# Kernel tuning notes

Hardware: AMD Instinct MI355X
Metric: run time of the kernel (lower is better)

The kernel has to match this reference:

```python
import jax, jax.numpy as jnp
import numpy as np

B, S, HID = 2, 2048, 4096
NH, NKV, D = 32, 8, 128
GROUPS = NH // NKV  # 4 query heads per KV head
THETA = 10000.0
MAX_SEQ = 4096


def _rope_tables():
    half = D // 2
    inv_freq = 1.0 / (THETA ** (np.arange(half, dtype=np.float32) / half))
    t = np.arange(MAX_SEQ, dtype=np.float32)
    freqs = np.outer(t, inv_freq)  # [MAX_SEQ, D//2]
    return jnp.asarray(np.cos(freqs)), jnp.asarray(np.sin(freqs))

ROPE_COS, ROPE_SIN = _rope_tables()


def _apply_rope(x, cos, sin):
    # x: [B, S, H, D]; cos/sin: [S, D//2]; half-split (NeoX) rotation as in _apply_rope_inline
    half = x.shape[-1] // 2
    x0, x1 = x[..., :half], x[..., half:]
    c = cos[None, :, None, :]
    s = sin[None, :, None, :]
    return jnp.concatenate([x0 * c - x1 * s, x0 * s + x1 * c], axis=-1)


def setup_inputs() -> dict:
    key = jax.random.key(0)
    ks = jax.random.split(key, 5)
    wscale = 1.0 / np.sqrt(HID).astype(np.float32)  # keep activations O(1)
    return {
        "x": jax.random.normal(ks[0], (B, S, HID), dtype=jnp.float32),
        "positions": jnp.arange(S, dtype=jnp.int32),
        "w_q": jax.random.normal(ks[1], (NH * D, HID), dtype=jnp.float32) * wscale,
        "w_k": jax.random.normal(ks[2], (NKV * D, HID), dtype=jnp.float32) * wscale,
        "w_v": jax.random.normal(ks[3], (NKV * D, HID), dtype=jnp.float32) * wscale,
        "w_o": jax.random.normal(ks[4], (HID, NH * D), dtype=jnp.float32) * wscale,
    }


def reference(x, positions, w_q, w_k, w_v, w_o):
    cos = ROPE_COS[positions]  # [S, D//2]
    sin = ROPE_SIN[positions]
    # Separate Q/K/V projections (no bias), as in the training forward()
    q = (x @ w_q.T).reshape(B, S, NH, D)
    k = (x @ w_k.T).reshape(B, S, NKV, D)
    v = (x @ w_v.T).reshape(B, S, NKV, D)
    q = _apply_rope(q, cos, sin)
    k = _apply_rope(k, cos, sin)
    # [B, H, S, D] layout
    q = q.transpose(0, 2, 1, 3)
    k = k.transpose(0, 2, 1, 3)
    v = v.transpose(0, 2, 1, 3)
    # GQA: group query heads over shared KV heads instead of repeating K/V
    qg = q.reshape(B, NKV, GROUPS, S, D)
    scale = 1.0 / jnp.sqrt(jnp.float32(D))
    scores = jnp.einsum("bkgqd,bkmd->bkgqm", qg, k) * scale  # [B, NKV, G, Sq, Skv]
    causal = jnp.tril(jnp.ones((S, S), dtype=bool))
    scores = jnp.where(causal[None, None, None], scores, jnp.float32(-jnp.inf))
    probs = jax.nn.softmax(scores, axis=-1)
    ctx = jnp.einsum("bkgqm,bkmd->bkgqd", probs, v)  # [B, NKV, G, S, D]
    ctx = ctx.reshape(B, NH, S, D).transpose(0, 2, 1, 3).reshape(B, S, NH * D)
    return ctx @ w_o.T
```

## Files before the change

### kernel.cpp

```cpp
#include <hip/hip_runtime.h>
#include <math.h>

typedef short s16x8 __attribute__((ext_vector_type(8)));
typedef float f32x4 __attribute__((ext_vector_type(4)));
typedef unsigned u32x4 __attribute__((ext_vector_type(4)));
typedef unsigned short u16;

#define S_LEN 2048
#define HID_DIM 4096
#define NH_Q 32
#define NKV_H 8
#define DHEAD 128

__device__ __forceinline__ u16 f2bf(float f) {
  unsigned u = __builtin_bit_cast(unsigned, f);
  u += 0x7fffu + ((u >> 16) & 1u);
  return (u16)(u >> 16);
}

__device__ __forceinline__ void gload16(const u16* g, u16* l) {
  __builtin_amdgcn_global_load_lds(
      (const __attribute__((address_space(1))) void*)g,
      (__attribute__((address_space(3))) void*)l, 16, 0, 0);
}

__global__ void cvt_kernel(const float* __restrict__ in, u16* __restrict__ out, int n4) {
  int stride = gridDim.x * blockDim.x;
  for (int i = blockIdx.x * blockDim.x + threadIdx.x; i < n4; i += stride) {
    float4 f = ((const float4*)in)[i];
    uint2 o;
    o.x = (unsigned)f2bf(f.x) | ((unsigned)f2bf(f.y) << 16);
    o.y = (unsigned)f2bf(f.z) | ((unsigned)f2bf(f.w) << 16);
    ((uint2*)out)[i] = o;
  }
}

__global__ void cvt_all_kernel(const float* __restrict__ x, const float* __restrict__ wq,
                               const float* __restrict__ wk, const float* __restrict__ wv,
                               const float* __restrict__ wo, u16* __restrict__ x_bf,
                               u16* __restrict__ wqkv_bf, u16* __restrict__ wo_bf,
                               int with_wo) {
  const int R0 = 4194304, R1 = 8388608, R2 = 9437184, R3 = 10485760, R4 = 14680064;
  const int total = with_wo ? R4 : R3;
  const int stride = gridDim.x * blockDim.x;
  for (int i = blockIdx.x * blockDim.x + threadIdx.x; i < total; i += stride) {
    const float* src;
    u16* dst;
    int off;
    if (i < R0)      { src = x;  dst = x_bf;               off = i; }
    else if (i < R1) { src = wq; dst = wqkv_bf;            off = i - R0; }
    else if (i < R2) { src = wk; dst = wqkv_bf + 16777216; off = i - R1; }
    else if (i < R3) { src = wv; dst = wqkv_bf + 20971520; off = i - R2; }
    else             { src = wo; dst = wo_bf;              off = i - R3; }
    float4 f = ((const float4*)src)[off];
    uint2 o;
    o.x = (unsigned)f2bf(f.x) | ((unsigned)f2bf(f.y) << 16);
    o.y = (unsigned)f2bf(f.z) | ((unsigned)f2bf(f.w) << 16);
    ((uint2*)dst)[off] = o;
  }
}

__global__ void rope_table_kernel(const int* __restrict__ positions,
                                  float* __restrict__ cos_t, float* __restrict__ sin_t) {
  int idx = blockIdx.x * 256 + threadIdx.x;
  if (idx >= S_LEN * 64) return;
  int s = idx >> 6, j = idx & 63;
  float pos = (float)positions[s];
  float inv = expf(-(float)j * (9.210340371976184f / 64.0f));
  float ang = pos * inv;
  float sv, cv;
  sincosf(ang, &sv, &cv);
  cos_t[idx] = cv;
  sin_t[idx] = sv;
}

template<int EPI>
__global__ __launch_bounds__(512, 2) void gemm8ph_kernel(
    const u16* __restrict__ A, const u16* __restrict__ B,
    void* __restrict__ outp, int M, int N, int K,
    const float* __restrict__ cos_t, const float* __restrict__ sin_t) {
  __shared__ u16 LDS[65536];
  const int t = threadIdx.x;
  const int wave = t >> 6, lane = t & 63;
  const int l15 = lane & 15, lhi = lane >> 4;
  const int wr = wave >> 2, wc = wave & 3;
  const int gx = gridDim.x;
  const int nwg = gx * gridDim.y;
  const int id = blockIdx.y * gx + blockIdx.x;
  const int swz = (id & 7) * (nwg >> 3) + (id >> 3);
  const int bm = (swz / gx) * 256, bn = (swz % gx) * 256;

  const int sw = l15 & 7;
  int aoff[4][2], boff[2][2];
#pragma unroll
  for (int q = 0; q < 4; ++q)
#pragma unroll
    for (int ks = 0; ks < 2; ++ks)
      aoff[q][ks] = (wr * 64 + q * 16 + l15) * 64 + (((ks << 2) + lhi) ^ sw) * 8;
#pragma unroll
  for (int f = 0; f < 2; ++f)
#pragma unroll
    for (int ks = 0; ks < 2; ++ks)
      boff[f][ks] = (f * 64 + wc * 16 + l15) * 64 + (((ks << 2) + lhi) ^ sw) * 8;

  const int lr1 = t >> 3;
  const int cs1 = ((t & 7) ^ (lr1 & 7)) * 8;
  const int rA1 = lr1;
  const int rA2 = 128 + lr1;
  const int ldsw = wave * 512;

  const f32x4 fz = {0.f, 0.f, 0.f, 0.f};
  f32x4 acc[8][4];
#pragma unroll
  for (int mf = 0; mf < 8; ++mf)
#pragma unroll
    for (int nf = 0; nf < 4; ++nf) acc[mf][nf] = fz;

  auto stageA = [&](int tile, int h, int buf) {
    const size_t kb = (size_t)tile * 64;
    gload16(A + (size_t)(bm + h * 64 + rA1) * K + kb + cs1,
            &LDS[buf * 16384 + h * 8192 + ldsw]);
    gload16(A + (size_t)(bm + h * 64 + rA2) * K + kb + cs1,
            &LDS[buf * 16384 + h * 8192 + 4096 + ldsw]);
  };
  auto stageB = [&](int tile, int h, int buf) {
    const size_t kb = (size_t)tile * 64;
    gload16(B + (size_t)(bn + h * 128 + lr1) * K + kb + cs1,
            &LDS[32768 + buf * 16384 + h * 8192 + ldsw]);
    gload16(B + (size_t)(bn + h * 128 + 64 + lr1) * K + kb + cs1,
            &LDS[32768 + buf * 16384 + h * 8192 + 4096 + ldsw]);
  };

  s16x8 afr[4][2], bfr[2][2], bfrK[2][2];
  auto readA = [&](int mfH, int buf) {
    const int base = buf * 16384 + mfH * 8192;
#pragma unroll
    for (int q = 0; q < 4; ++q)
#pragma unroll
      for (int ks = 0; ks < 2; ++ks)
        afr[q][ks] = *(const s16x8*)&LDS[base + aoff[q][ks]];
  };
  auto readB = [&](int nfH, int buf, s16x8 (&dst)[2][2]) {
    const int base = 32768 + buf * 16384 + nfH * 8192;
#pragma unroll
    for (int f = 0; f < 2; ++f)
#pragma unroll
      for (int ks = 0; ks < 2; ++ks)
        dst[f][ks] = *(const s16x8*)&LDS[base + boff[f][ks]];
  };
  auto mfma16 = [&](int mfH, int nfH, const s16x8 (&bb)[2][2]) {
    __builtin_amdgcn_s_setprio(1);
#pragma unroll
    for (int q = 0; q < 4; ++q)
#pragma unroll
      for (int f = 0; f < 2; ++f)
#pragma unroll
        for (int ks = 0; ks < 2; ++ks)
          acc[mfH * 4 + q][nfH * 2 + f] = __builtin_amdgcn_mfma_f32_16x16x32_bf16(
              afr[q][ks], bb[f][ks], acc[mfH * 4 + q][nfH * 2 + f], 0, 0, 0);
    __builtin_amdgcn_s_setprio(0);
  };

#define PHASE_SYNC()                        \
  do {                                      \
    __builtin_amdgcn_s_barrier();           \
    asm volatile("s_waitcnt lgkmcnt(0)");   \
    __builtin_amdgcn_sched_barrier(0);      \
  } while (0)

  stageA(0, 0, 0); stageB(0, 0, 0); stageB(0, 1, 0); stageA(0, 1, 0);
  stageA(1, 0, 1); stageB(1, 0, 1); stageB(1, 1, 1);
  asm volatile("s_waitcnt vmcnt(6)");
  __builtin_amdgcn_sched_barrier(0);
  __builtin_amdgcn_s_barrier();

  const int nt = K >> 6;
  for (int i = 0; i < (nt >> 1); ++i) {
    const int u = 2 * i, v = 2 * i + 1;
    const bool s2 = (u + 2) < nt;
    readA(0, 0); readB(0, 0, bfrK); stageA(v, 1, 1);
    PHASE_SYNC(); mfma16(0, 0, bfrK); __builtin_amdgcn_s_barrier();
    readB(1, 0, bfr); if (s2) stageB(u + 2, 0, 0);
    PHASE_SYNC(); mfma16(0, 1, bfr); __builtin_amdgcn_s_barrier();
    readA(1, 0); if (s2) stageB(u + 2, 1, 0);
    PHASE_SYNC(); mfma16(1, 1, bfr); __builtin_amdgcn_s_barrier();
    if (s2) { stageA(u + 2, 0, 0); asm volatile("s_waitcnt vmcnt(6)"); }
    else    { asm volatile("s_waitcnt vmcnt(0)"); }
    PHASE_SYNC(); mfma16(1, 0, bfrK); __builtin_amdgcn_s_barrier();
    readA(0, 1); readB(0, 1, bfrK); if (s2) stageA(u + 2, 1, 0);
    PHASE_SYNC(); mfma16(0, 0, bfrK); __builtin_amdgcn_s_barrier();
    readB(1, 1, bfr); if (s2) stageB(v + 2, 0, 1);
    PHASE_SYNC(); mfma16(0, 1, bfr); __builtin_amdgcn_s_barrier();
    readA(1, 1); if (s2) stageB(v + 2, 1, 1);
    PHASE_SYNC(); mfma16(1, 1, bfr); __builtin_amdgcn_s_barrier();
    if (s2) { stageA(v + 2, 0, 1); asm volatile("s_waitcnt vmcnt(6)"); }
    else    { asm volatile("s_waitcnt vmcnt(0)"); }
    PHASE_SYNC(); mfma16(1, 0, bfrK); __builtin_amdgcn_s_barrier();
  }
#undef PHASE_SYNC

  if constexpr (EPI == 0) {
    float* C = (float*)outp;
#pragma unroll
    for (int mf = 0; mf < 8; ++mf) {
      int rb = bm + wr * 128 + mf * 16 + lhi * 4;
#pragma unroll
      for (int nfi = 0; nfi < 4; ++nfi) {
        int col = bn + wc * 16 + (nfi & 1) * 64 + (nfi >> 1) * 128 + l15;
#pragma unroll
        for (int i = 0; i < 4; ++i) C[(size_t)(rb + i) * N + col] = acc[mf][nfi][i];
      }
    }
  } else {
    u16* qp = (u16*)outp;
    u16* kp = qp + 16777216;
    u16* vp = kp + 4194304;
    if (bn < 5120) {
      const bool isQ = bn < 4096;
      u16* O = isQ ? qp : kp;
      const int hb = isQ ? (bn >> 7) : ((bn - 4096) >> 7);
      const int Hh = isQ ? NH_Q : NKV_H;
      const int j = wc * 16 + l15;
#pragma unroll
      for (int mf = 0; mf < 8; ++mf) {
        int rb = bm + wr * 128 + mf * 16 + lhi * 4;
#pragma unroll
        for (int p = 0; p < 2; ++p) {
          int head = hb + p;
#pragma unroll
          for (int i = 0; i < 4; ++i) {
            int m = rb + i;
            int b = m >> 11, srw = m & 2047;
            float c = cos_t[srw * 64 + j];
            float s = sin_t[srw * 64 + j];
            float x0 = acc[mf][2 * p][i];
            float x1 = acc[mf][2 * p + 1][i];
            size_t base = ((size_t)(b * Hh + head) * S_LEN + srw) * DHEAD;
            O[base + j] = f2bf(x0 * c - x1 * s);
            O[base + j + 64] = f2bf(x0 * s + x1 * c);
          }
        }
      }
    } else {
#pragma unroll
      for (int mf = 0; mf < 8; ++mf) {
        int rb = bm + wr * 128 + mf * 16 + lhi * 4;
#pragma unroll
        for (int nfi = 0; nfi < 4; ++nfi) {
          int colrel = bn - 5120 + wc * 16 + (nfi & 1) * 64 + (nfi >> 1) * 128 + l15;
          int head = colrel >> 7, d = colrel & 127;
#pragma unroll
          for (int i = 0; i < 4; ++i) {
            int m = rb + i;
            int b = m >> 11, srw = m & 2047;
            vp[((size_t)(b * NKV_H + head) * DHEAD + d) * S_LEN + srw] = f2bf(acc[mf][nfi][i]);
          }
        }
      }
    }
  }
}

template<int EPI, bool ABF16, bool BBF16>
__global__ __launch_bounds__(256) void gemm_kernel(
    const void* __restrict__ Aptr, const void* __restrict__ Bptr,
    void* __restrict__ outp, void* __restrict__ outp2, int M, int N, int K,
    const float* __restrict__ cos_t, const float* __restrict__ sin_t, int Hh) {
  __shared__ u16 As[128][72];
  __shared__ u16 Bs[128][72];
  const int t = threadIdx.x;
  const int wave = t >> 6, lane = t & 63;
  const int l15 = lane & 15, lhi = lane >> 4;
  const int gx = gridDim.x;
  const int nwg = gx * gridDim.y;
  const int id = blockIdx.y * gx + blockIdx.x;
  const int swz = (id & 7) * (nwg >> 3) + (id >> 3);
  const int bm = (swz / gx) * 128, bn = (swz % gx) * 128;

  const f32x4 fz = {0.f, 0.f, 0.f, 0.f};
  f32x4 acc[2][8];
#pragma unroll
  for (int a0 = 0; a0 < 2; ++a0)
#pragma unroll
    for (int b0 = 0; b0 < 8; ++b0) acc[a0][b0] = fz;

  for (int kt = 0; kt < K; kt += 64) {
    __syncthreads();
    if (ABF16) {
      const u16* A = (const u16*)Aptr;
#pragma unroll
      for (int p = 0; p < 4; ++p) {
        int row = p * 32 + (t >> 3), kc = (t & 7) * 8;
        *(s16x8*)&As[row][kc] = *(const s16x8*)(A + (size_t)(bm + row) * K + kt + kc);
      }
    } else {
      const float* A = (const float*)Aptr;
#pragma unroll
      for (int p = 0; p < 8; ++p) {
        int row = p * 16 + (t >> 4), kc = (t & 15) * 4;
        float4 f = *(const float4*)(A + (size_t)(bm + row) * K + kt + kc);
        unsigned* dst = (unsigned*)&As[row][kc];
        dst[0] = (unsigned)f2bf(f.x) | ((unsigned)f2bf(f.y) << 16);
        dst[1] = (unsigned)f2bf(f.z) | ((unsigned)f2bf(f.w) << 16);
      }
    }
    if (BBF16) {
      const u16* Bw = (const u16*)Bptr;
#pragma unroll
      for (int p = 0; p < 4; ++p) {
        int row = p * 32 + (t >> 3), kc = (t & 7) * 8;
        *(s16x8*)&Bs[row][kc] = *(const s16x8*)(Bw + (size_t)(bn + row) * K + kt + kc);
      }
    } else {
      const float* Bw = (const float*)Bptr;
#pragma unroll
      for (int p = 0; p < 8; ++p) {
        int row = p * 16 + (t >> 4), kc = (t & 15) * 4;
        float4 f = *(const float4*)(Bw + (size_t)(bn + row) * K + kt + kc);
        unsigned* dst = (unsigned*)&Bs[row][kc];
        dst[0] = (unsigned)f2bf(f.x) | ((unsigned)f2bf(f.y) << 16);
        dst[1] = (unsigned)f2bf(f.z) | ((unsigned)f2bf(f.w) << 16);
      }
    }
    __syncthreads();
#pragma unroll
    for (int ks = 0; ks < 2; ++ks) {
      s16x8 bfr[8];
#pragma unroll
      for (int nf = 0; nf < 8; ++nf)
        bfr[nf] = *(const s16x8*)&Bs[nf * 16 + l15][ks * 32 + lhi * 8];
#pragma unroll
      for (int mf = 0; mf < 2; ++mf) {
        s16x8 a = *(const s16x8*)&As[wave * 32 + mf * 16 + l15][ks * 32 + lhi * 8];
#pragma unroll
        for (int nf = 0; nf < 8; ++nf)
          acc[mf][nf] = __builtin_amdgcn_mfma_f32_16x16x32_bf16(a, bfr[nf], acc[mf][nf], 0, 0, 0);
      }
    }
  }

  if (EPI == 0) {
    float* C = (float*)outp;
#pragma unroll
    for (int mf = 0; mf < 2; ++mf)
#pragma unroll
      for (int nf = 0; nf < 8; ++nf) {
        int col = bn + nf * 16 + l15;
        int rb = bm + wave * 32 + mf * 16 + lhi * 4;
#pragma unroll
        for (int i = 0; i < 4; ++i) C[(size_t)(rb + i) * N + col] = acc[mf][nf][i];
      }
  } else if (EPI == 2) {
    u16* O = (u16*)outp;
    int h = bn >> 7;
#pragma unroll
    for (int mf = 0; mf < 2; ++mf)
#pragma unroll
      for (int nf = 0; nf < 4; ++nf) {
        int j = nf * 16 + l15;
        int rb = bm + wave * 32 + mf * 16 + lhi * 4;
#pragma unroll
        for (int i = 0; i < 4; ++i) {
          int m = rb + i;
          int b = m >> 11, srow = m & 2047;
          float c = cos_t[srow * 64 + j];
          float s = sin_t[srow * 64 + j];
          float x0 = acc[mf][nf][i];
          float x1 = acc[mf][nf + 4][i];
          size_t base = ((size_t)(b * Hh + h) * S_LEN + srow) * DHEAD;
          O[base + j] = f2bf(x0 * c - x1 * s);
          O[base + j + 64] = f2bf(x0 * s + x1 * c);
        }
      }
  } else {
    u16* O = (u16*)outp;
#pragma unroll
    for (int mf = 0; mf < 2; ++mf)
#pragma unroll
      for (int nf = 0; nf < 8; ++nf) {
        int col = bn + nf * 16 + l15;
        int h = col >> 7, d = col & 127;
        int rb = bm + wave * 32 + mf * 16 + lhi * 4;
#pragma unroll
        for (int i = 0; i < 4; ++i) {
          int m = rb + i;
          int b = m >> 11, srow = m & 2047;
          O[((size_t)(b * Hh + h) * DHEAD + d) * S_LEN + srow] = f2bf(acc[mf][nf][i]);
        }
      }
  }
}

#define KIDX(r, c) (((r) * 128 + (c)) ^ (((r) & 7) << 3))
#define VIDX(d, kv) (((d) * 64 + (kv)) ^ (((d) & 7) << 3))
__global__ __launch_bounds__(512) void attn_kernel(
    const u16* __restrict__ q, const u16* __restrict__ k, const u16* __restrict__ vt,
    u16* __restrict__ ctx) {
  __shared__ u16 Ks[64 * 128];
  __shared__ u16 Vts[128 * 64];

  const int t = threadIdx.x;
  const int wave = t >> 6, lane = t & 63;
  const int l15 = lane & 15, lhi = lane >> 4;
  const int pi = blockIdx.x, h = blockIdx.y, b = blockIdx.z;
  const int kvh = h >> 2;
  const int qsub[2] = {pi, 15 - pi};
  const int ntiles = 32 - 2 * pi;

  const u16* qb = q + ((size_t)(b * NH_Q + h)) * S_LEN * DHEAD;
  const u16* kb = k + ((size_t)(b * NKV_H + kvh)) * S_LEN * DHEAD;
  const u16* vtb = vt + ((size_t)(b * NKV_H + kvh)) * DHEAD * S_LEN;
// ... 45 lines not shown
      kr0 = *(const s16x8*)p;
      kr1 = *(const s16x8*)(p + 8);
      const u16* pv = vtb + (size_t)vrow * S_LEN + (tt + 1) * 64 + vk0;
      vr0 = *(const s16x8*)pv;
      vr1 = *(const s16x8*)(pv + 8);
    }

    const int kc_base = tt * 64;
#pragma unroll
    for (int s = 0; s < 2; ++s) {
      const int wmin = qsub[s] * 128 + wave * 16;
      if (kc_base > wmin + 15) continue;
      f32x4 sacc[4];
#pragma unroll
      for (int i = 0; i < 4; ++i) sacc[i] = fz;
      __builtin_amdgcn_s_setprio(1);
#pragma unroll
      for (int ks = 0; ks < 4; ++ks) {
#pragma unroll
        for (int nf = 0; nf < 4; ++nf) {
          s16x8 kf = *(const s16x8*)&Ks[KIDX(nf * 16 + l15, ks * 32 + lhi * 8)];
          sacc[nf] = __builtin_amdgcn_mfma_f32_16x16x32_bf16(kf, qf[s][ks], sacc[nf], 0, 0, 0);
        }
      }
      __builtin_amdgcn_s_setprio(0);

      const int qg = wmin + l15;
      float pmax = -INFINITY;
      if (kc_base + 63 > wmin) {
#pragma unroll
        for (int nf = 0; nf < 4; ++nf)
#pragma unroll
          for (int i = 0; i < 4; ++i) {
            int kv = kc_base + nf * 16 + lhi * 4 + i;
            float sv = sacc[nf][i] * scale;
            sv = (kv <= qg) ? sv : -INFINITY;
            sacc[nf][i] = sv;
            pmax = fmaxf(pmax, sv);
          }
      } else {
#pragma unroll
        for (int nf = 0; nf < 4; ++nf)
#pragma unroll
          for (int i = 0; i < 4; ++i) {
            float sv = sacc[nf][i] * scale;
            sacc[nf][i] = sv;
            pmax = fmaxf(pmax, sv);
          }
      }
      pmax = fmaxf(pmax, __shfl_xor(pmax, 16, 64));
      pmax = fmaxf(pmax, __shfl_xor(pmax, 32, 64));

      if (!__all(pmax <= mrow[s] + 8.0f)) {
        float mnew = fmaxf(mrow[s], pmax);
        float alpha = __expf(mrow[s] - mnew);
        mrow[s] = mnew;
        lsum[s] *= alpha;
#pragma unroll
        for (int i = 0; i < 4; ++i) {
          float al = __shfl(alpha, (lane & 48) | (lhi * 4 + i), 64);
#pragma unroll
          for (int df = 0; df < 8; ++df) acc[s][df][i] *= al;
        }
      }

      float rsum = 0.f;
      unsigned pk[4][2];
#pragma unroll
      for (int nf = 0; nf < 4; ++nf) {
        float p0 = __expf(sacc[nf][0] - mrow[s]);
        float p1 = __expf(sacc[nf][1] - mrow[s]);
        float p2 = __expf(sacc[nf][2] - mrow[s]);
        float p3 = __expf(sacc[nf][3] - mrow[s]);
        rsum += (p0 + p1) + (p2 + p3);
        pk[nf][0] = (unsigned)f2bf(p0) | ((unsigned)f2bf(p1) << 16);
        pk[nf][1] = (unsigned)f2bf(p2) | ((unsigned)f2bf(p3) << 16);
      }
      rsum += __shfl_xor(rsum, 16, 64);
      rsum += __shfl_xor(rsum, 32, 64);
      lsum[s] += rsum;

      s16x8 pa[2];
#pragma unroll
      for (int ph = 0; ph < 2; ++ph) {
        unsigned lo0 = __shfl((int)pk[2 * ph][0], sl0, 64);
        unsigned hi0 = __shfl((int)pk[2 * ph + 1][0], sl0, 64);
        unsigned lo1 = __shfl((int)pk[2 * ph][1], sl0, 64);
        unsigned hi1 = __shfl((int)pk[2 * ph + 1][1], sl0, 64);
        unsigned lo2 = __shfl((int)pk[2 * ph][0], sl1, 64);
        unsigned hi2 = __shfl((int)pk[2 * ph + 1][0], sl1, 64);
        unsigned lo3 = __shfl((int)pk[2 * ph][1], sl1, 64);
        unsigned hi3 = __shfl((int)pk[2 * ph + 1][1], sl1, 64);
        u32x4 w;
        w[0] = hisel ? hi0 : lo0;
        w[1] = hisel ? hi1 : lo1;
        w[2] = hisel ? hi2 : lo2;
        w[3] = hisel ? hi3 : lo3;
        pa[ph] = __builtin_bit_cast(s16x8, w);
      }

      __builtin_amdgcn_s_setprio(1);
#pragma unroll
      for (int ph = 0; ph < 2; ++ph) {
#pragma unroll
        for (int df = 0; df < 8; ++df) {
          s16x8 bb = *(const s16x8*)&Vts[VIDX(df * 16 + l15, ph * 32 + lhi * 8)];
          acc[s][df] = __builtin_amdgcn_mfma_f32_16x16x32_bf16(pa[ph], bb, acc[s][df], 0, 0, 0);
        }
      }
      __builtin_amdgcn_s_setprio(0);
    }
  }

#pragma unroll
  for (int s = 0; s < 2; ++s) {
    float rl = 1.0f / lsum[s];
#pragma unroll
    for (int i = 0; i < 4; ++i) {
      float rli = __shfl(rl, (lane & 48) | (lhi * 4 + i), 64);
      int m = b * S_LEN + qsub[s] * 128 + wave * 16 + lhi * 4 + i;
#pragma unroll
      for (int df = 0; df < 8; ++df) {
        int col = h * DHEAD + df * 16 + l15;
        ctx[(size_t)m * (NH_Q * DHEAD) + col] = f2bf(acc[s][df][i] * rli);
      }
    }
  }
}

extern "C" void kernel_launch(void* const* d_in, const int* in_sizes, int n_in,
                              void* d_out, int out_size, void* d_ws, size_t ws_size,
                              hipStream_t stream) {
  const float* x = (const float*)d_in[0];
  const int* positions = (const int*)d_in[1];
  const float* wq = (const float*)d_in[2];
  const float* wk = (const float*)d_in[3];
  const float* wv = (const float*)d_in[4];
  const float* wo = (const float*)d_in[5];
  float* out = (float*)d_out;

  char* ws = (char*)d_ws;
  const size_t MB1 = 1048576;
  const size_t SZ_X = 33554432;
  const size_t SZ_WQKV = 50331648;
  const size_t SZ_WO = 33554432;
  const size_t SZ_Q = 33554432;
  const size_t SZ_WK = 8388608;
  const size_t NEED_FULL = MB1 + SZ_X + SZ_WQKV + SZ_Q + 2 * SZ_WK;
  const size_t NEED_WO = NEED_FULL + SZ_WO;

  float* cos_t = (float*)ws;
  float* sin_t = (float*)(ws + MB1 / 2);

  rope_table_kernel<<<512, 256, 0, stream>>>(positions, cos_t, sin_t);

  if (ws_size >= NEED_WO) {
    char* p = ws + MB1;
    u16* x_bf = (u16*)p;    p += SZ_X;
    u16* wqkv_bf = (u16*)p; p += SZ_WQKV;
    u16* wo_bf = (u16*)p;   p += SZ_WO;
    u16* q_ws = (u16*)p;    p += SZ_Q;
    u16* k_ws = (u16*)p;    p += SZ_WK;
    u16* v_ws = (u16*)p;    p += SZ_WK;
    u16* ctx_ws = x_bf;

    cvt_all_kernel<<<2048, 256, 0, stream>>>(x, wq, wk, wv, wo, x_bf, wqkv_bf, wo_bf, 1);
    gemm8ph_kernel<5><<<dim3(24, 16), 512, 0, stream>>>(
        x_bf, wqkv_bf, q_ws, 4096, 6144, 4096, cos_t, sin_t);
    attn_kernel<<<dim3(8, 32, 2), 512, 0, stream>>>(q_ws, k_ws, v_ws, ctx_ws);
    gemm8ph_kernel<0><<<dim3(16, 16), 512, 0, stream>>>(
        ctx_ws, wo_bf, out, 4096, 4096, 4096, nullptr, nullptr);
  } else if (ws_size >= NEED_FULL) {
    char* p = ws + MB1;
    u16* x_bf = (u16*)p;    p += SZ_X;
    u16* wqkv_bf = (u16*)p; p += SZ_WQKV;
    u16* q_ws = (u16*)p;    p += SZ_Q;
    u16* k_ws = (u16*)p;    p += SZ_WK;
    u16* v_ws = (u16*)p;    p += SZ_WK;
    u16* ctx_ws = x_bf;

    cvt_all_kernel<<<2048, 256, 0, stream>>>(x, wq, wk, wv, nullptr, x_bf, wqkv_bf, nullptr, 0);
    gemm8ph_kernel<5><<<dim3(24, 16), 512, 0, stream>>>(
        x_bf, wqkv_bf, q_ws, 4096, 6144, 4096, cos_t, sin_t);
    cvt_kernel<<<2048, 256, 0, stream>>>(wo, wqkv_bf, 4194304);
    attn_kernel<<<dim3(8, 32, 2), 512, 0, stream>>>(q_ws, k_ws, v_ws, ctx_ws);
    gemm8ph_kernel<0><<<dim3(16, 16), 512, 0, stream>>>(
        ctx_ws, wqkv_bf, out, 4096, 4096, 4096, nullptr, nullptr);
  } else {
    u16* q_ws = (u16*)(ws + MB1);
    u16* k_ws = (u16*)(ws + MB1 + SZ_Q);
    u16* v_ws = (u16*)(ws + MB1 + SZ_Q + SZ_WK);
    u16* ctx_ws = (u16*)(ws + MB1 + SZ_Q + 2 * SZ_WK);

    gemm_kernel<2, false, false><<<dim3(32, 32), 256, 0, stream>>>(
        x, wq, q_ws, nullptr, 4096, 4096, 4096, cos_t, sin_t, NH_Q);
    gemm_kernel<2, false, false><<<dim3(8, 32), 256, 0, stream>>>(
        x, wk, k_ws, nullptr, 4096, 1024, 4096, cos_t, sin_t, NKV_H);
    gemm_kernel<4, false, false><<<dim3(8, 32), 256, 0, stream>>>(
        x, wv, v_ws, nullptr, 4096, 1024, 4096, nullptr, nullptr, NKV_H);
    attn_kernel<<<dim3(8, 32, 2), 512, 0, stream>>>(q_ws, k_ws, v_ws, ctx_ws);
    gemm_kernel<0, true, false><<<dim3(32, 32), 256, 0, stream>>>(
        ctx_ws, wo, out, nullptr, 4096, 4096, 4096, nullptr, nullptr, 0);
  }
}
```

Before: 537.1 us.

## Use 128x256-tile QKV GEMM kernel and fold RoPE table into conversion

Adds a dedicated QKV projection kernel that uses 128x256 output tiles with a three-stage LDS ring buffer, replacing the 256x256 eight-phase kernel. This doubles the grid to 768 workgroups so the MI355X compute units get a fuller wave of work. The RoPE cos/sin table generation moves into the bf16 conversion kernel, removing one launch. In exchange, smaller tiles give less operand reuse per workgroup and raise global/LDS traffic per FLOP.

New measurement: 525.3 us. 2.2% less time.

```diff
diff --git a/kernel.cpp b/kernel.cpp
--- a/kernel.cpp
+++ b/kernel.cpp
@@ -39,24 +39,42 @@
                                const float* __restrict__ wk, const float* __restrict__ wv,
                                const float* __restrict__ wo, u16* __restrict__ x_bf,
                                u16* __restrict__ wqkv_bf, u16* __restrict__ wo_bf,
-                               int with_wo) {
+                               const int* __restrict__ positions, float* __restrict__ cos_t,
+                               float* __restrict__ sin_t, int with_wo) {
   const int R0 = 4194304, R1 = 8388608, R2 = 9437184, R3 = 10485760, R4 = 14680064;
-  const int total = with_wo ? R4 : R3;
+  const int cvt_end = with_wo ? R4 : R3;
+  const int rope_units = 32768;
+  const int total = cvt_end + rope_units;
   const int stride = gridDim.x * blockDim.x;
   for (int i = blockIdx.x * blockDim.x + threadIdx.x; i < total; i += stride) {
-    const float* src;
-    u16* dst;
-    int off;
-    if (i < R0)      { src = x;  dst = x_bf;               off = i; }
-    else if (i < R1) { src = wq; dst = wqkv_bf;            off = i - R0; }
-    else if (i < R2) { src = wk; dst = wqkv_bf + 16777216; off = i - R1; }
-    else if (i < R3) { src = wv; dst = wqkv_bf + 20971520; off = i - R2; }
-    else             { src = wo; dst = wo_bf;              off = i - R3; }
-    float4 f = ((const float4*)src)[off];
-    uint2 o;
-    o.x = (unsigned)f2bf(f.x) | ((unsigned)f2bf(f.y) << 16);
-    o.y = (unsigned)f2bf(f.z) | ((unsigned)f2bf(f.w) << 16);
-    ((uint2*)dst)[off] = o;
+    if (i < cvt_end) {
+      const float* src;
+      u16* dst;
+      int off;
+      if (i < R0)      { src = x;  dst = x_bf;               off = i; }
+      else if (i < R1) { src = wq; dst = wqkv_bf;            off = i - R0; }
+      else if (i < R2) { src = wk; dst = wqkv_bf + 16777216; off = i - R1; }
+      else if (i < R3) { src = wv; dst = wqkv_bf + 20971520; off = i - R2; }
+      else             { src = wo; dst = wo_bf;              off = i - R3; }
+      float4 f = ((const float4*)src)[off];
+      uint2 o;
+      o.x = (unsigned)f2bf(f.x) | ((unsigned)f2bf(f.y) << 16);
+      o.y = (unsigned)f2bf(f.z) | ((unsigned)f2bf(f.w) << 16);
+      ((uint2*)dst)[off] = o;
+    } else {
+      int base = (i - cvt_end) * 4;
+#pragma unroll
+      for (int e = 0; e < 4; ++e) {
+        int idx = base + e;
+        int s = idx >> 6, j = idx & 63;
+        float pos = (float)positions[s];
+        float inv = expf(-(float)j * (9.210340371976184f / 64.0f));
+        float sv, cv;
+        sincosf(pos * inv, &sv, &cv);
+        cos_t[idx] = cv;
+        sin_t[idx] = sv;
+      }
+    }
   }
 }
 
@@ -67,18 +85,174 @@
   int s = idx >> 6, j = idx & 63;
   float pos = (float)positions[s];
   float inv = expf(-(float)j * (9.210340371976184f / 64.0f));
-  float ang = pos * inv;
   float sv, cv;
-  sincosf(ang, &sv, &cv);
+  sincosf(pos * inv, &sv, &cv);
   cos_t[idx] = cv;
   sin_t[idx] = sv;
 }
 
-template<int EPI>
-__global__ __launch_bounds__(512, 2) void gemm8ph_kernel(
+__global__ __launch_bounds__(512, 2) void gemmq_kernel(
     const u16* __restrict__ A, const u16* __restrict__ B,
     void* __restrict__ outp, int M, int N, int K,
     const float* __restrict__ cos_t, const float* __restrict__ sin_t) {
+  __shared__ u16 LDS[73728];
+  const int t = threadIdx.x;
+  const int wave = t >> 6, lane = t & 63;
+  const int l15 = lane & 15, lhi = lane >> 4;
+  const int wr = wave >> 2, wc = wave & 3;
+  const int gx = gridDim.x;
+  const int nwg = gx * gridDim.y;
+  const int id = blockIdx.y * gx + blockIdx.x;
+  const int swz = (id & 7) * (nwg >> 3) + (id >> 3);
+  const int bm = (swz / gx) * 128, bn = (swz % gx) * 256;
+
+  const int sw = l15 & 7;
+  int aoff[4][2], boff[2][2];
+#pragma unroll
+  for (int q = 0; q < 4; ++q)
+#pragma unroll
+    for (int ks = 0; ks < 2; ++ks)
+      aoff[q][ks] = wr * 4096 + (q * 16 + l15) * 64 + (((ks << 2) + lhi) ^ sw) * 8;
+#pragma unroll
+  for (int f = 0; f < 2; ++f)
+#pragma unroll
+    for (int ks = 0; ks < 2; ++ks)
+      boff[f][ks] = (f * 64 + wc * 16 + l15) * 64 + (((ks << 2) + lhi) ^ sw) * 8;
+
+  const int lr1 = t >> 3;
+  const int cs1 = ((t & 7) ^ (lr1 & 7)) * 8;
+  const int ldsw = wave * 512;
+
+  const f32x4 fz = {0.f, 0.f, 0.f, 0.f};
+  f32x4 acc[4][4];
+#pragma unroll
+  for (int mf = 0; mf < 4; ++mf)
+#pragma unroll
+    for (int nf = 0; nf < 4; ++nf) acc[mf][nf] = fz;
+
+  auto stageA = [&](int tile, int buf) {
+    const size_t kb = (size_t)tile * 64;
+    gload16(A + (size_t)(bm + lr1) * K + kb + cs1, &LDS[buf * 8192 + ldsw]);
+    gload16(A + (size_t)(bm + 64 + lr1) * K + kb + cs1, &LDS[buf * 8192 + 4096 + ldsw]);
+  };
+  auto stageB = [&](int tile, int h, int buf) {
+    const size_t kb = (size_t)tile * 64;
+    gload16(B + (size_t)(bn + h * 128 + lr1) * K + kb + cs1,
+            &LDS[24576 + buf * 16384 + h * 8192 + ldsw]);
+    gload16(B + (size_t)(bn + h * 128 + 64 + lr1) * K + kb + cs1,
+            &LDS[24576 + buf * 16384 + h * 8192 + 4096 + ldsw]);
+  };
+
+  s16x8 afr[4][2], bfr[2][2];
+  auto readA = [&](int buf) {
+    const int base = buf * 8192;
+#pragma unroll
+    for (int q = 0; q < 4; ++q)
+#pragma unroll
+      for (int ks = 0; ks < 2; ++ks)
+        afr[q][ks] = *(const s16x8*)&LDS[base + aoff[q][ks]];
+  };
+  auto readB = [&](int nfH, int buf) {
+    const int base = 24576 + buf * 16384 + nfH * 8192;
+#pragma unroll
+    for (int f = 0; f < 2; ++f)
+#pragma unroll
+      for (int ks = 0; ks < 2; ++ks)
+        bfr[f][ks] = *(const s16x8*)&LDS[base + boff[f][ks]];
+  };
+  auto mfma16 = [&](int nfH) {
+    __builtin_amdgcn_s_setprio(1);
+#pragma unroll
+    for (int q = 0; q < 4; ++q)
+#pragma unroll
+      for (int f = 0; f < 2; ++f)
+#pragma unroll
+        for (int ks = 0; ks < 2; ++ks)
+          acc[q][nfH * 2 + f] = __builtin_amdgcn_mfma_f32_16x16x32_bf16(
+              afr[q][ks], bfr[f][ks], acc[q][nfH * 2 + f], 0, 0, 0);
+    __builtin_amdgcn_s_setprio(0);
+  };
+
+#define PHASE_SYNC()                        \
+  do {                                      \
+    __builtin_amdgcn_s_barrier();           \
+    asm volatile("s_waitcnt lgkmcnt(0)");   \
+    __builtin_amdgcn_sched_barrier(0);      \
+  } while (0)
+
+  stageA(0, 0); stageB(0, 0, 0); stageB(0, 1, 0);
+  stageA(1, 1); stageB(1, 0, 1); stageB(1, 1, 1);
+  asm volatile("s_waitcnt vmcnt(6)");
+  __builtin_amdgcn_sched_barrier(0);
+  __builtin_amdgcn_s_barrier();
+
+  const int nt = K >> 6;
+  int cur = 0, nx2 = 2;
+  for (int tt = 0; tt < nt; ++tt) {
+    const bool s2 = (tt + 2) < nt;
+    readA(cur); readB(0, cur);
+    if (s2) { stageA(tt + 2, nx2); stageB(tt + 2, 0, nx2); }
+    PHASE_SYNC(); mfma16(0); __builtin_amdgcn_s_barrier();
+    readB(1, cur);
+    if (s2) { stageB(tt + 2, 1, nx2); asm volatile("s_waitcnt vmcnt(6)"); }
+    else    { asm volatile("s_waitcnt vmcnt(0)"); }
+    PHASE_SYNC(); mfma16(1); __builtin_amdgcn_s_barrier();
+    cur = (cur == 2) ? 0 : cur + 1;
+    nx2 = (nx2 == 2) ? 0 : nx2 + 1;
+  }
+#undef PHASE_SYNC
+
+  u16* qp = (u16*)outp;
+  u16* kp = qp + 16777216;
+  u16* vp = kp + 4194304;
+  if (bn < 5120) {
+    const bool isQ = bn < 4096;
+    u16* O = isQ ? qp : kp;
+    const int hb = isQ ? (bn >> 7) : ((bn - 4096) >> 7);
+    const int Hh = isQ ? NH_Q : NKV_H;
+    const int j = wc * 16 + l15;
+#pragma unroll
+    for (int mf = 0; mf < 4; ++mf) {
+      int rb = bm + wr * 64 + mf * 16 + lhi * 4;
+#pragma unroll
+      for (int p = 0; p < 2; ++p) {
+        int head = hb + p;
+#pragma unroll
+        for (int i = 0; i < 4; ++i) {
+          int m = rb + i;
+          int b = m >> 11, srw = m & 2047;
+          float c = cos_t[srw * 64 + j];
+          float s = sin_t[srw * 64 + j];
+          float x0 = acc[mf][2 * p][i];
+          float x1 = acc[mf][2 * p + 1][i];
+          size_t base = ((size_t)(b * Hh + head) * S_LEN + srw) * DHEAD;
+          O[base + j] = f2bf(x0 * c - x1 * s);
+          O[base + j + 64] = f2bf(x0 * s + x1 * c);
+        }
+      }
+    }
+  } else {
+#pragma unroll
+    for (int mf = 0; mf < 4; ++mf) {
+      int rb = bm + wr * 64 + mf * 16 + lhi * 4;
+#pragma unroll
+      for (int nfi = 0; nfi < 4; ++nfi) {
+        int colrel = bn - 5120 + wc * 16 + (nfi & 1) * 64 + (nfi >> 1) * 128 + l15;
+        int head = colrel >> 7, d = colrel & 127;
+#pragma unroll
+        for (int i = 0; i < 4; ++i) {
+          int m = rb + i;
+          int b = m >> 11, srw = m & 2047;
+          vp[((size_t)(b * NKV_H + head) * DHEAD + d) * S_LEN + srw] = f2bf(acc[mf][nfi][i]);
+        }
+      }
+    }
+  }
+}
+
+__global__ __launch_bounds__(512, 2) void gemm8ph_kernel(
+    const u16* __restrict__ A, const u16* __restrict__ B,
+    void* __restrict__ outp, int M, int N, int K) {
   __shared__ u16 LDS[65536];
   const int t = threadIdx.x;
   const int wave = t >> 6, lane = t & 63;
@@ -199,64 +373,15 @@
   }
 #undef PHASE_SYNC
 
-  if constexpr (EPI == 0) {
-    float* C = (float*)outp;
-#pragma unroll
-    for (int mf = 0; mf < 8; ++mf) {
-      int rb = bm + wr * 128 + mf * 16 + lhi * 4;
-#pragma unroll
-      for (int nfi = 0; nfi < 4; ++nfi) {
-        int col = bn + wc * 16 + (nfi & 1) * 64 + (nfi >> 1) * 128 + l15;
-#pragma unroll
-        for (int i = 0; i < 4; ++i) C[(size_t)(rb + i) * N + col] = acc[mf][nfi][i];
-      }
-    }
-  } else {
-    u16* qp = (u16*)outp;
-    u16* kp = qp + 16777216;
-    u16* vp = kp + 4194304;
-    if (bn < 5120) {
-      const bool isQ = bn < 4096;
-      u16* O = isQ ? qp : kp;
-      const int hb = isQ ? (bn >> 7) : ((bn - 4096) >> 7);
-      const int Hh = isQ ? NH_Q : NKV_H;
-      const int j = wc * 16 + l15;
-#pragma unroll
-      for (int mf = 0; mf < 8; ++mf) {
-        int rb = bm + wr * 128 + mf * 16 + lhi * 4;
-#pragma unroll
-        for (int p = 0; p < 2; ++p) {
-          int head = hb + p;
-#pragma unroll
-          for (int i = 0; i < 4; ++i) {
-            int m = rb + i;
-            int b = m >> 11, srw = m & 2047;
-            float c = cos_t[srw * 64 + j];
-            float s = sin_t[srw * 64 + j];
-            float x0 = acc[mf][2 * p][i];
-            float x1 = acc[mf][2 * p + 1][i];
-            size_t base = ((size_t)(b * Hh + head) * S_LEN + srw) * DHEAD;
-            O[base + j] = f2bf(x0 * c - x1 * s);
-            O[base + j + 64] = f2bf(x0 * s + x1 * c);
-          }
-        }
-      }
-    } else {
-#pragma unroll
-      for (int mf = 0; mf < 8; ++mf) {
-        int rb = bm + wr * 128 + mf * 16 + lhi * 4;
-#pragma unroll
-        for (int nfi = 0; nfi < 4; ++nfi) {
-          int colrel = bn - 5120 + wc * 16 + (nfi & 1) * 64 + (nfi >> 1) * 128 + l15;
-          int head = colrel >> 7, d = colrel & 127;
-#pragma unroll
-          for (int i = 0; i < 4; ++i) {
-            int m = rb + i;
-            int b = m >> 11, srw = m & 2047;
-            vp[((size_t)(b * NKV_H + head) * DHEAD + d) * S_LEN + srw] = f2bf(acc[mf][nfi][i]);
-          }
-        }
-      }
+  float* C = (float*)outp;
+#pragma unroll
+  for (int mf = 0; mf < 8; ++mf) {
+    int rb = bm + wr * 128 + mf * 16 + lhi * 4;
+#pragma unroll
+    for (int nfi = 0; nfi < 4; ++nfi) {
+      int col = bn + wc * 16 + (nfi & 1) * 64 + (nfi >> 1) * 128 + l15;
+#pragma unroll
+      for (int i = 0; i < 4; ++i) C[(size_t)(rb + i) * N + col] = acc[mf][nfi][i];
     }
   }
 }
@@ -608,8 +733,6 @@
   float* cos_t = (float*)ws;
   float* sin_t = (float*)(ws + MB1 / 2);
 
-  rope_table_kernel<<<512, 256, 0, stream>>>(positions, cos_t, sin_t);
-
   if (ws_size >= NEED_WO) {
     char* p = ws + MB1;
     u16* x_bf = (u16*)p;    p += SZ_X;
@@ -620,12 +743,13 @@
     u16* v_ws = (u16*)p;    p += SZ_WK;
     u16* ctx_ws = x_bf;
 
-    cvt_all_kernel<<<2048, 256, 0, stream>>>(x, wq, wk, wv, wo, x_bf, wqkv_bf, wo_bf, 1);
-    gemm8ph_kernel<5><<<dim3(24, 16), 512, 0, stream>>>(
+    cvt_all_kernel<<<2048, 256, 0, stream>>>(x, wq, wk, wv, wo, x_bf, wqkv_bf, wo_bf,
+                                             positions, cos_t, sin_t, 1);
+    gemmq_kernel<<<dim3(24, 32), 512, 0, stream>>>(
         x_bf, wqkv_bf, q_ws, 4096, 6144, 4096, cos_t, sin_t);
     attn_kernel<<<dim3(8, 32, 2), 512, 0, stream>>>(q_ws, k_ws, v_ws, ctx_ws);
-    gemm8ph_kernel<0><<<dim3(16, 16), 512, 0, stream>>>(
-        ctx_ws, wo_bf, out, 4096, 4096, 4096, nullptr, nullptr);
+    gemm8ph_kernel<<<dim3(16, 16), 512, 0, stream>>>(
+        ctx_ws, wo_bf, out, 4096, 4096, 4096);
   } else if (ws_size >= NEED_FULL) {
     char* p = ws + MB1;
     u16* x_bf = (u16*)p;    p += SZ_X;
@@ -635,19 +759,21 @@
     u16* v_ws = (u16*)p;    p += SZ_WK;
     u16* ctx_ws = x_bf;
 
-    cvt_all_kernel<<<2048, 256, 0, stream>>>(x, wq, wk, wv, nullptr, x_bf, wqkv_bf, nullptr, 0);
-    gemm8ph_kernel<5><<<dim3(24, 16), 512, 0, stream>>>(
+    cvt_all_kernel<<<2048, 256, 0, stream>>>(x, wq, wk, wv, nullptr, x_bf, wqkv_bf, nullptr,
+                                             positions, cos_t, sin_t, 0);
+    gemmq_kernel<<<dim3(24, 32), 512, 0, stream>>>(
         x_bf, wqkv_bf, q_ws, 4096, 6144, 4096, cos_t, sin_t);
     cvt_kernel<<<2048, 256, 0, stream>>>(wo, wqkv_bf, 4194304);
     attn_kernel<<<dim3(8, 32, 2), 512, 0, stream>>>(q_ws, k_ws, v_ws, ctx_ws);
-    gemm8ph_kernel<0><<<dim3(16, 16), 512, 0, stream>>>(
-        ctx_ws, wqkv_bf, out, 4096, 4096, 4096, nullptr, nullptr);
+    gemm8ph_kernel<<<dim3(16, 16), 512, 0, stream>>>(
+        ctx_ws, wqkv_bf, out, 4096, 4096, 4096);
   } else {
     u16* q_ws = (u16*)(ws + MB1);
     u16* k_ws = (u16*)(ws + MB1 + SZ_Q);
     u16* v_ws = (u16*)(ws + MB1 + SZ_Q + SZ_WK);
     u16* ctx_ws = (u16*)(ws + MB1 + SZ_Q + 2 * SZ_WK);
 
+    rope_table_kernel<<<512, 256, 0, stream>>>(positions, cos_t, sin_t);
     gemm_kernel<2, false, false><<<dim3(32, 32), 256, 0, stream>>>(
         x, wq, q_ws, nullptr, 4096, 4096, 4096, cos_t, sin_t, NH_Q);
     gemm_kernel<2, false, false><<<dim3(8, 32), 256, 0, stream>>>(
```

## Shrink GEMM tile to 128x256, triple-buffer LDS pipeline, fuse RoPE table into convert

Applied to the files above, without the earlier changes.

Shrinks the bf16 GEMM block tile from 256x256 to 128x256, which doubles the grid. It replaces the eight-phase barrier schedule with a triple-buffered LDS pipeline that double-buffers register fragments, so each k-tile needs one barrier. The RoPE cos/sin table computation moves into the dtype-conversion kernel, removing one launch. Smaller tiles raise occupancy and wave count but lower arithmetic intensity per block and add global traffic.

Result: no change. 532.9 us (-0.8%).

```diff
diff --git a/kernel.cpp b/kernel.cpp
--- a/kernel.cpp
+++ b/kernel.cpp
@@ -39,24 +39,42 @@
                                const float* __restrict__ wk, const float* __restrict__ wv,
                                const float* __restrict__ wo, u16* __restrict__ x_bf,
                                u16* __restrict__ wqkv_bf, u16* __restrict__ wo_bf,
-                               int with_wo) {
+                               const int* __restrict__ positions, float* __restrict__ cos_t,
+                               float* __restrict__ sin_t, int with_wo) {
   const int R0 = 4194304, R1 = 8388608, R2 = 9437184, R3 = 10485760, R4 = 14680064;
-  const int total = with_wo ? R4 : R3;
+  const int cvt_end = with_wo ? R4 : R3;
+  const int rope_units = 32768;
+  const int total = cvt_end + rope_units;
   const int stride = gridDim.x * blockDim.x;
   for (int i = blockIdx.x * blockDim.x + threadIdx.x; i < total; i += stride) {
-    const float* src;
-    u16* dst;
-    int off;
-    if (i < R0)      { src = x;  dst = x_bf;               off = i; }
-    else if (i < R1) { src = wq; dst = wqkv_bf;            off = i - R0; }
-    else if (i < R2) { src = wk; dst = wqkv_bf + 16777216; off = i - R1; }
-    else if (i < R3) { src = wv; dst = wqkv_bf + 20971520; off = i - R2; }
-    else             { src = wo; dst = wo_bf;              off = i - R3; }
-    float4 f = ((const float4*)src)[off];
-    uint2 o;
-    o.x = (unsigned)f2bf(f.x) | ((unsigned)f2bf(f.y) << 16);
-    o.y = (unsigned)f2bf(f.z) | ((unsigned)f2bf(f.w) << 16);
-    ((uint2*)dst)[off] = o;
+    if (i < cvt_end) {
+      const float* src;
+      u16* dst;
+      int off;
+      if (i < R0)      { src = x;  dst = x_bf;               off = i; }
+      else if (i < R1) { src = wq; dst = wqkv_bf;            off = i - R0; }
+      else if (i < R2) { src = wk; dst = wqkv_bf + 16777216; off = i - R1; }
+      else if (i < R3) { src = wv; dst = wqkv_bf + 20971520; off = i - R2; }
+      else             { src = wo; dst = wo_bf;              off = i - R3; }
+      float4 f = ((const float4*)src)[off];
+      uint2 o;
+      o.x = (unsigned)f2bf(f.x) | ((unsigned)f2bf(f.y) << 16);
+      o.y = (unsigned)f2bf(f.z) | ((unsigned)f2bf(f.w) << 16);
+      ((uint2*)dst)[off] = o;
+    } else {
+      int base = (i - cvt_end) * 4;
+#pragma unroll
+      for (int e = 0; e < 4; ++e) {
+        int idx = base + e;
+        int s = idx >> 6, j = idx & 63;
+        float pos = (float)positions[s];
+        float inv = expf(-(float)j * (9.210340371976184f / 64.0f));
+        float sv, cv;
+        sincosf(pos * inv, &sv, &cv);
+        cos_t[idx] = cv;
+        sin_t[idx] = sv;
+      }
+    }
   }
 }
 
@@ -67,19 +85,18 @@
   int s = idx >> 6, j = idx & 63;
   float pos = (float)positions[s];
   float inv = expf(-(float)j * (9.210340371976184f / 64.0f));
-  float ang = pos * inv;
   float sv, cv;
-  sincosf(ang, &sv, &cv);
+  sincosf(pos * inv, &sv, &cv);
   cos_t[idx] = cv;
   sin_t[idx] = sv;
 }
 
 template<int EPI>
-__global__ __launch_bounds__(512, 2) void gemm8ph_kernel(
+__global__ __launch_bounds__(512, 2) void gemmp_kernel(
     const u16* __restrict__ A, const u16* __restrict__ B,
     void* __restrict__ outp, int M, int N, int K,
     const float* __restrict__ cos_t, const float* __restrict__ sin_t) {
-  __shared__ u16 LDS[65536];
+  __shared__ u16 LDS[73728];
   const int t = threadIdx.x;
   const int wave = t >> 6, lane = t & 63;
   const int l15 = lane & 15, lhi = lane >> 4;
@@ -88,7 +105,7 @@
   const int nwg = gx * gridDim.y;
   const int id = blockIdx.y * gx + blockIdx.x;
   const int swz = (id & 7) * (nwg >> 3) + (id >> 3);
-  const int bm = (swz / gx) * 256, bn = (swz % gx) * 256;
+  const int bm = (swz / gx) * 128, bn = (swz % gx) * 256;
 
   const int sw = l15 & 7;
   int aoff[4][2], boff[2][2];
@@ -96,7 +113,7 @@
   for (int q = 0; q < 4; ++q)
 #pragma unroll
     for (int ks = 0; ks < 2; ++ks)
-      aoff[q][ks] = (wr * 64 + q * 16 + l15) * 64 + (((ks << 2) + lhi) ^ sw) * 8;
+      aoff[q][ks] = wr * 4096 + (q * 16 + l15) * 64 + (((ks << 2) + lhi) ^ sw) * 8;
 #pragma unroll
   for (int f = 0; f < 2; ++f)
 #pragma unroll
@@ -105,105 +122,106 @@
 
   const int lr1 = t >> 3;
   const int cs1 = ((t & 7) ^ (lr1 & 7)) * 8;
-  const int rA1 = lr1;
-  const int rA2 = 128 + lr1;
   const int ldsw = wave * 512;
 
   const f32x4 fz = {0.f, 0.f, 0.f, 0.f};
-  f32x4 acc[8][4];
-#pragma unroll
-  for (int mf = 0; mf < 8; ++mf)
+  f32x4 acc[4][4];
+#pragma unroll
+  for (int mf = 0; mf < 4; ++mf)
 #pragma unroll
     for (int nf = 0; nf < 4; ++nf) acc[mf][nf] = fz;
 
-  auto stageA = [&](int tile, int h, int buf) {
+  auto stageA = [&](int tile, int buf) {
     const size_t kb = (size_t)tile * 64;
-    gload16(A + (size_t)(bm + h * 64 + rA1) * K + kb + cs1,
-            &LDS[buf * 16384 + h * 8192 + ldsw]);
-    gload16(A + (size_t)(bm + h * 64 + rA2) * K + kb + cs1,
-            &LDS[buf * 16384 + h * 8192 + 4096 + ldsw]);
+    gload16(A + (size_t)(bm + lr1) * K + kb + cs1, &LDS[buf * 8192 + ldsw]);
+    gload16(A + (size_t)(bm + 64 + lr1) * K + kb + cs1, &LDS[buf * 8192 + 4096 + ldsw]);
   };
   auto stageB = [&](int tile, int h, int buf) {
     const size_t kb = (size_t)tile * 64;
     gload16(B + (size_t)(bn + h * 128 + lr1) * K + kb + cs1,
-            &LDS[32768 + buf * 16384 + h * 8192 + ldsw]);
+            &LDS[24576 + buf * 16384 + h * 8192 + ldsw]);
     gload16(B + (size_t)(bn + h * 128 + 64 + lr1) * K + kb + cs1,
-            &LDS[32768 + buf * 16384 + h * 8192 + 4096 + ldsw]);
+            &LDS[24576 + buf * 16384 + h * 8192 + 4096 + ldsw]);
   };
 
-  s16x8 afr[4][2], bfr[2][2], bfrK[2][2];
-  auto readA = [&](int mfH, int buf) {
-    const int base = buf * 16384 + mfH * 8192;
-#pragma unroll
-    for (int q = 0; q < 4; ++q)
-#pragma unroll
-      for (int ks = 0; ks < 2; ++ks)
-        afr[q][ks] = *(const s16x8*)&LDS[base + aoff[q][ks]];
-  };
-  auto readB = [&](int nfH, int buf, s16x8 (&dst)[2][2]) {
-    const int base = 32768 + buf * 16384 + nfH * 8192;
-#pragma unroll
-    for (int f = 0; f < 2; ++f)
-#pragma unroll
-      for (int ks = 0; ks < 2; ++ks)
-        dst[f][ks] = *(const s16x8*)&LDS[base + boff[f][ks]];
-  };
-  auto mfma16 = [&](int mfH, int nfH, const s16x8 (&bb)[2][2]) {
-    __builtin_amdgcn_s_setprio(1);
-#pragma unroll
-    for (int q = 0; q < 4; ++q)
-#pragma unroll
-      for (int f = 0; f < 2; ++f)
-#pragma unroll
-        for (int ks = 0; ks < 2; ++ks)
-          acc[mfH * 4 + q][nfH * 2 + f] = __builtin_amdgcn_mfma_f32_16x16x32_bf16(
-              afr[q][ks], bb[f][ks], acc[mfH * 4 + q][nfH * 2 + f], 0, 0, 0);
-    __builtin_amdgcn_s_setprio(0);
-  };
-
-#define PHASE_SYNC()                        \
-  do {                                      \
-    __builtin_amdgcn_s_barrier();           \
-    asm volatile("s_waitcnt lgkmcnt(0)");   \
-    __builtin_amdgcn_sched_barrier(0);      \
+  s16x8 afr0[4][2], afr1[4][2];
+  s16x8 bfr00[2][2], bfr01[2][2];
+  s16x8 bfr10[2][2], bfr11[2][2];
+
+#define READ_TILE(SET, BUF)                                                \
+  do {                                                                     \
+    const int _b = (BUF);                                                  \
+    const int _ba = _b * 8192;                                             \
+    _Pragma("unroll") for (int q = 0; q < 4; ++q)                          \
+      _Pragma("unroll") for (int ks = 0; ks < 2; ++ks)                     \
+        afr##SET[q][ks] = *(const s16x8*)&LDS[_ba + aoff[q][ks]];          \
+    const int _b0 = 24576 + _b * 16384;                                    \
+    _Pragma("unroll") for (int f = 0; f < 2; ++f)                          \
+      _Pragma("unroll") for (int ks = 0; ks < 2; ++ks)                     \
+        bfr0##SET[f][ks] = *(const s16x8*)&LDS[_b0 + boff[f][ks]];         \
+    const int _b1 = _b0 + 8192;                                            \
+    _Pragma("unroll") for (int f = 0; f < 2; ++f)                          \
+      _Pragma("unroll") for (int ks = 0; ks < 2; ++ks)                     \
+        bfr1##SET[f][ks] = *(const s16x8*)&LDS[_b1 + boff[f][ks]];         \
   } while (0)
 
-  stageA(0, 0, 0); stageB(0, 0, 0); stageB(0, 1, 0); stageA(0, 1, 0);
-  stageA(1, 0, 1); stageB(1, 0, 1); stageB(1, 1, 1);
-  asm volatile("s_waitcnt vmcnt(6)");
+#define MFMA_HALF(SET, NFH, BH)                                            \
+  do {                                                                     \
+    __builtin_amdgcn_s_setprio(1);                                         \
+    _Pragma("unroll") for (int q = 0; q < 4; ++q)                          \
+      _Pragma("unroll") for (int f = 0; f < 2; ++f)                        \
+        _Pragma("unroll") for (int ks = 0; ks < 2; ++ks)                   \
+          acc[q][(NFH)*2 + f] = __builtin_amdgcn_mfma_f32_16x16x32_bf16(   \
+              afr##SET[q][ks], bfr##BH##SET[f][ks], acc[q][(NFH)*2 + f],   \
+              0, 0, 0);                                                    \
+    __builtin_amdgcn_s_setprio(0);                                         \
+  } while (0)
+
+#define TILE_BODY(SET, OSET, TT)                                           \
+  do {                                                                     \
+    const int _tt = (TT);                                                  \
+    const bool _s2 = _tt + 2 < nt;                                         \
+    if (_s2) { stageA(_tt + 2, nx2); stageB(_tt + 2, 0, nx2); }            \
+    asm volatile("s_waitcnt lgkmcnt(0)" ::: "memory");                     \
+    __builtin_amdgcn_sched_barrier(0);                                     \
+    MFMA_HALF(SET, 0, 0);                                                  \
+    if (_s2) stageB(_tt + 2, 1, nx2);                                      \
+    if (_tt + 1 < nt) {                                                    \
+      if (_s2) { asm volatile("s_waitcnt vmcnt(6)" ::: "memory"); }        \
+      else     { asm volatile("s_waitcnt vmcnt(0)" ::: "memory"); }        \
+      __builtin_amdgcn_sched_barrier(0);                                   \
+      __builtin_amdgcn_s_barrier();                                        \
+      __builtin_amdgcn_sched_barrier(0);                                   \
+      READ_TILE(OSET, nxt1);                                               \
+    }                                                                      \
+    MFMA_HALF(SET, 1, 1);                                                  \
+    nxt1 = nx2;                                                            \
+    nx2 = (nx2 == 2) ? 0 : nx2 + 1;                                        \
+  } while (0)
+
+  const int nt = K >> 6;
+  stageA(0, 0); stageB(0, 0, 0); stageB(0, 1, 0);
+  stageA(1, 1); stageB(1, 0, 1); stageB(1, 1, 1);
+  asm volatile("s_waitcnt vmcnt(6)" ::: "memory");
   __builtin_amdgcn_sched_barrier(0);
   __builtin_amdgcn_s_barrier();
-
-  const int nt = K >> 6;
-  for (int i = 0; i < (nt >> 1); ++i) {
-    const int u = 2 * i, v = 2 * i + 1;
-    const bool s2 = (u + 2) < nt;
-    readA(0, 0); readB(0, 0, bfrK); stageA(v, 1, 1);
-    PHASE_SYNC(); mfma16(0, 0, bfrK); __builtin_amdgcn_s_barrier();
-    readB(1, 0, bfr); if (s2) stageB(u + 2, 0, 0);
-    PHASE_SYNC(); mfma16(0, 1, bfr); __builtin_amdgcn_s_barrier();
-    readA(1, 0); if (s2) stageB(u + 2, 1, 0);
-    PHASE_SYNC(); mfma16(1, 1, bfr); __builtin_amdgcn_s_barrier();
-    if (s2) { stageA(u + 2, 0, 0); asm volatile("s_waitcnt vmcnt(6)"); }
-    else    { asm volatile("s_waitcnt vmcnt(0)"); }
-    PHASE_SYNC(); mfma16(1, 0, bfrK); __builtin_amdgcn_s_barrier();
-    readA(0, 1); readB(0, 1, bfrK); if (s2) stageA(u + 2, 1, 0);
-    PHASE_SYNC(); mfma16(0, 0, bfrK); __builtin_amdgcn_s_barrier();
-    readB(1, 1, bfr); if (s2) stageB(v + 2, 0, 1);
-    PHASE_SYNC(); mfma16(0, 1, bfr); __builtin_amdgcn_s_barrier();
-    readA(1, 1); if (s2) stageB(v + 2, 1, 1);
-    PHASE_SYNC(); mfma16(1, 1, bfr); __builtin_amdgcn_s_barrier();
-    if (s2) { stageA(v + 2, 0, 1); asm volatile("s_waitcnt vmcnt(6)"); }
-    else    { asm volatile("s_waitcnt vmcnt(0)"); }
-    PHASE_SYNC(); mfma16(1, 0, bfrK); __builtin_amdgcn_s_barrier();
-  }
-#undef PHASE_SYNC
+  __builtin_amdgcn_sched_barrier(0);
+  READ_TILE(0, 0);
+
+  int nxt1 = 1, nx2 = 2;
+  for (int tt = 0; tt < nt; tt += 2) {
+    TILE_BODY(0, 1, tt);
+    TILE_BODY(1, 0, tt + 1);
+  }
+#undef TILE_BODY
+#undef MFMA_HALF
+#undef READ_TILE
 
   if constexpr (EPI == 0) {
     float* C = (float*)outp;
 #pragma unroll
-    for (int mf = 0; mf < 8; ++mf) {
-      int rb = bm + wr * 128 + mf * 16 + lhi * 4;
+    for (int mf = 0; mf < 4; ++mf) {
+      int rb = bm + wr * 64 + mf * 16 + lhi * 4;
 #pragma unroll
       for (int nfi = 0; nfi < 4; ++nfi) {
         int col = bn + wc * 16 + (nfi & 1) * 64 + (nfi >> 1) * 128 + l15;
@@ -222,8 +240,8 @@
       const int Hh = isQ ? NH_Q : NKV_H;
       const int j = wc * 16 + l15;
 #pragma unroll
-      for (int mf = 0; mf < 8; ++mf) {
-        int rb = bm + wr * 128 + mf * 16 + lhi * 4;
+      for (int mf = 0; mf < 4; ++mf) {
+        int rb = bm + wr * 64 + mf * 16 + lhi * 4;
 #pragma unroll
         for (int p = 0; p < 2; ++p) {
           int head = hb + p;
@@ -243,8 +261,8 @@
       }
     } else {
 #pragma unroll
-      for (int mf = 0; mf < 8; ++mf) {
-        int rb = bm + wr * 128 + mf * 16 + lhi * 4;
+      for (int mf = 0; mf < 4; ++mf) {
+        int rb = bm + wr * 64 + mf * 16 + lhi * 4;
 #pragma unroll
         for (int nfi = 0; nfi < 4; ++nfi) {
           int colrel = bn - 5120 + wc * 16 + (nfi & 1) * 64 + (nfi >> 1) * 128 + l15;
@@ -608,8 +626,6 @@
   float* cos_t = (float*)ws;
   float* sin_t = (float*)(ws + MB1 / 2);
 
-  rope_table_kernel<<<512, 256, 0, stream>>>(positions, cos_t, sin_t);
-
   if (ws_size >= NEED_WO) {
     char* p = ws + MB1;
     u16* x_bf = (u16*)p;    p += SZ_X;
@@ -620,11 +636,12 @@
     u16* v_ws = (u16*)p;    p += SZ_WK;
     u16* ctx_ws = x_bf;
 
-    cvt_all_kernel<<<2048, 256, 0, stream>>>(x, wq, wk, wv, wo, x_bf, wqkv_bf, wo_bf, 1);
-    gemm8ph_kernel<5><<<dim3(24, 16), 512, 0, stream>>>(
+    cvt_all_kernel<<<2048, 256, 0, stream>>>(x, wq, wk, wv, wo, x_bf, wqkv_bf, wo_bf,
+                                             positions, cos_t, sin_t, 1);
+    gemmp_kernel<5><<<dim3(24, 32), 512, 0, stream>>>(
         x_bf, wqkv_bf, q_ws, 4096, 6144, 4096, cos_t, sin_t);
     attn_kernel<<<dim3(8, 32, 2), 512, 0, stream>>>(q_ws, k_ws, v_ws, ctx_ws);
-    gemm8ph_kernel<0><<<dim3(16, 16), 512, 0, stream>>>(
+    gemmp_kernel<0><<<dim3(16, 32), 512, 0, stream>>>(
         ctx_ws, wo_bf, out, 4096, 4096, 4096, nullptr, nullptr);
   } else if (ws_size >= NEED_FULL) {
     char* p = ws + MB1;
@@ -635,12 +652,13 @@
     u16* v_ws = (u16*)p;    p += SZ_WK;
     u16* ctx_ws = x_bf;
 
-    cvt_all_kernel<<<2048, 256, 0, stream>>>(x, wq, wk, wv, nullptr, x_bf, wqkv_bf, nullptr, 0);
-    gemm8ph_kernel<5><<<dim3(24, 16), 512, 0, stream>>>(
+    cvt_all_kernel<<<2048, 256, 0, stream>>>(x, wq, wk, wv, nullptr, x_bf, wqkv_bf, nullptr,
+                                             positions, cos_t, sin_t, 0);
+    gemmp_kernel<5><<<dim3(24, 32), 512, 0, stream>>>(
         x_bf, wqkv_bf, q_ws, 4096, 6144, 4096, cos_t, sin_t);
     cvt_kernel<<<2048, 256, 0, stream>>>(wo, wqkv_bf, 4194304);
     attn_kernel<<<dim3(8, 32, 2), 512, 0, stream>>>(q_ws, k_ws, v_ws, ctx_ws);
-    gemm8ph_kernel<0><<<dim3(16, 16), 512, 0, stream>>>(
+    gemmp_kernel<0><<<dim3(16, 32), 512, 0, stream>>>(
         ctx_ws, wqkv_bf, out, 4096, 4096, 4096, nullptr, nullptr);
   } else {
     u16* q_ws = (u16*)(ws + MB1);
@@ -648,6 +666,7 @@
     u16* v_ws = (u16*)(ws + MB1 + SZ_Q + SZ_WK);
     u16* ctx_ws = (u16*)(ws + MB1 + SZ_Q + 2 * SZ_WK);
 
+    rope_table_kernel<<<512, 256, 0, stream>>>(positions, cos_t, sin_t);
     gemm_kernel<2, false, false><<<dim3(32, 32), 256, 0, stream>>>(
         x, wq, q_ws, nullptr, 4096, 4096, 4096, cos_t, sin_t, NH_Q);
     gemm_kernel<2, false, false><<<dim3(8, 32), 256, 0, stream>>>(
```
